# Kernel tuning notes

Measured on AMD Instinct MI355X. Metric: run time of the kernel, lower is better.

Reference implementation:

```python
import jax, jax.numpy as jnp
import numpy as np

D = 16      # input_dim (state dimension)
H = 64      # hidden width
B = 32768   # batch size


def setup_inputs() -> dict:
    key = jax.random.key(0)
    ks = jax.random.split(key, 16)
    inp = {
        "ts": jnp.arange(3, dtype=jnp.float32),          # output times [0, 1, 2]
        "x0": jax.random.normal(ks[0], (B, D), jnp.float32),
    }
    dims = [(D, H), (H, H), (H, H), (H, D)]
    i = 1
    for l, (din, dout) in enumerate(dims):
        inp[f"W{l}"] = jax.random.normal(ks[i], (din, dout), jnp.float32) / np.sqrt(din).astype(np.float32)
        inp[f"b{l}"] = jnp.zeros((dout,), jnp.float32)
        inp[f"g{l}"] = jax.random.normal(ks[i + 1], (dout,), jnp.float32) * 0.1   # hyper_gate weight (Linear(1,dout))
        inp[f"gb{l}"] = jnp.zeros((dout,), jnp.float32)                            # hyper_gate bias
        inp[f"hb{l}"] = jax.random.normal(ks[i + 2], (dout,), jnp.float32) * 0.1   # hyper_bias weight (no bias)
        i += 3
    return inp


def reference(ts, x0,
              W0, b0, g0, gb0, hb0,
              W1, b1, g1, gb1, hb1,
              W2, b2, g2, gb2, hb2,
              W3, b3, g3, gb3, hb3):
    layers = [(W0, b0, g0, gb0, hb0), (W1, b1, g1, gb1, hb1),
              (W2, b2, g2, gb2, hb2), (W3, b3, g3, gb3, hb3)]
    n_layers = len(layers)

    def odenet(t, x):
        # ConcatSquashLinear: (x@W + b) * sigmoid(t*g + gb) + t*hb, tanh between layers
        h = x
        for l, (W, b, g, gb, hb) in enumerate(layers):
            h = (h @ W + b) * jax.nn.sigmoid(t * g + gb) + t * hb
            if l < n_layers - 1:
                h = jnp.tanh(h)
        return h

    def odefunc(t, z):
        # z: [B, D+2]; last two channels accumulate log-det and kinetic energy
        x = z[:, :D]
        f = lambda xx: odenet(t, xx)
        dx = f(x)
        # exact divergence = trace of Jacobian, via D forward-mode JVPs
        eye = jnp.eye(D, dtype=x.dtype)
        Jv = jax.vmap(lambda e: jax.jvp(f, (x,), (jnp.broadcast_to(e, x.shape),))[1])(eye)  # [D, B, D]
        dl = jnp.einsum('ibi->b', Jv)                  # trace per sample
        dv = 0.5 * jnp.sum(dx * dx, axis=1)            # kinetic energy density
        return jnp.concatenate([dx, dl[:, None], dv[:, None]], axis=1)

    z0 = jnp.pad(x0, ((0, 0), (0, 2)))  # F.pad(x0, (0,2)) with zeros

    def rk4_step(z, t_pair):
        t0, t1 = t_pair
        h = t1 - t0
        k1 = odefunc(t0, z)
        k2 = odefunc(t0 + 0.5 * h, z + 0.5 * h * k1)
        k3 = odefunc(t0 + 0.5 * h, z + 0.5 * h * k2)
        k4 = odefunc(t1, z + h * k3)
        zn = z + (h / 6.0) * (k1 + 2.0 * k2 + 2.0 * k3 + k4)
        return zn, zn

    _, zs_tail = jax.lax.scan(rk4_step, z0, (ts[:-1], ts[1:]))
    zs = jnp.concatenate([z0[None], zs_tail], axis=0)   # [T, B, D+2]

    xs = zs[:, :, :-2]
    log_det = zs[-1, :, -2]
    loss_L = jnp.abs(zs[-1, :, -1])
    return xs, log_det, loss_L, jnp.zeros_like(loss_L)
```

## Files before the change

kernel.cpp:

```cpp
#include <hip/hip_runtime.h>

#define NB 32768
#define DD 16
#define HH 64
#define EPB 16

typedef __attribute__((ext_vector_type(8))) short short8;
typedef __attribute__((ext_vector_type(2))) float f32x2;
typedef __attribute__((ext_vector_type(4))) float f32x4;
typedef __attribute__((ext_vector_type(4))) unsigned uint4v;

union Frag { short8 s; uint4v u; unsigned d[4]; };

struct Params {
  const float *ts, *x0;
  const float *W0,*b0,*g0,*gb0,*hb0;
  const float *W1,*b1,*g1,*gb1,*hb1;
  const float *W2,*b2,*g2,*gb2,*hb2;
  const float *W3,*b3,*g3,*gb3,*hb3;
  float *out;
};

__device__ __forceinline__ unsigned short f2bf(float f){
  unsigned u=__float_as_uint(f);
  return (unsigned short)((u + 0x7FFFu + ((u>>16)&1u))>>16);
}
__device__ __forceinline__ unsigned pk2bf(float lo, float hi){
  unsigned a=__float_as_uint(lo)+0x8000u;
  unsigned b=__float_as_uint(hi)+0x8000u;
  return __builtin_amdgcn_perm(b, a, 0x07060302u);
}
__device__ __forceinline__ unsigned pk2bf2(f32x2 v){
  unsigned a=__float_as_uint(v[0])+0x8000u;
  unsigned b=__float_as_uint(v[1])+0x8000u;
  return __builtin_amdgcn_perm(b, a, 0x07060302u);
}
__device__ __forceinline__ unsigned short f2bf1(float f){
  return (unsigned short)((__float_as_uint(f)+0x8000u)>>16);
}
__device__ __forceinline__ float sigm(float u){
  return __builtin_amdgcn_rcpf(1.0f+__builtin_amdgcn_exp2f(-1.44269504f*u));
}
#define WV() __builtin_amdgcn_wave_barrier()
#define MFMA(A,B,C) __builtin_amdgcn_mfma_f32_16x16x32_bf16((A),(B),(C),0,0,0)

__device__ __forceinline__ void fwd_epi(const f32x4& c, float tcur,
    float gc, float gbc, float hbc,
    unsigned short* __restrict__ hdst, float* __restrict__ sdst,
    int jw, int q)
{
  const float gate = sigm(tcur*gc+gbc);
  const float gk   = gate*2.88539008f;
  const float tbk  = (tcur*hbc)*2.88539008f;
  const float g4   = 4.0f*gate;
  const f32x2 c01={c[0],c[1]}, c23={c[2],c[3]};
  const f32x2 pre01 = c01*gk + tbk;
  const f32x2 pre23 = c23*gk + tbk;
  const f32x2 e01={__builtin_amdgcn_exp2f(pre01[0]),__builtin_amdgcn_exp2f(pre01[1])};
  const f32x2 e23={__builtin_amdgcn_exp2f(pre23[0]),__builtin_amdgcn_exp2f(pre23[1])};
  const f32x2 d01=e01+1.0f, d23=e23+1.0f;
  const f32x2 rc01={__builtin_amdgcn_rcpf(d01[0]),__builtin_amdgcn_rcpf(d01[1])};
  const f32x2 rc23={__builtin_amdgcn_rcpf(d23[0]),__builtin_amdgcn_rcpf(d23[1])};
  const f32x2 th01 = rc01*-2.0f + 1.0f;
  const f32x2 th23 = rc23*-2.0f + 1.0f;
  const f32x2 om01 = 1.0f - rc01, om23 = 1.0f - rc23;
  const f32x2 sv01 = (rc01*g4)*om01, sv23 = (rc23*g4)*om23;
  const int el0=q*4;
  hdst[(el0+0)*72+jw]=f2bf1(th01[0]);
  hdst[(el0+1)*72+jw]=f2bf1(th01[1]);
  hdst[(el0+2)*72+jw]=f2bf1(th23[0]);
  hdst[(el0+3)*72+jw]=f2bf1(th23[1]);
  sdst[(el0+0)*68+jw]=sv01[0];
  sdst[(el0+1)*68+jw]=sv01[1];
  sdst[(el0+2)*68+jw]=sv23[0];
  sdst[(el0+3)*68+jw]=sv23[1];
}

__global__ __launch_bounds__(256,2) void traj_kernel(Params p){
  __shared__ __align__(16) unsigned short w0b[DD][72];
  __shared__ __align__(16) float w3tt[HH][20];
  __shared__ __align__(16) unsigned short xh[DD][40];
  __shared__ __align__(16) unsigned short xl[DD][40];
  __shared__ __align__(16) unsigned short hbh[2][EPB][72];
  __shared__ __align__(16) float sbf[3][EPB][68];
  __shared__ __align__(16) float sig3w[4][DD];
  __shared__ __align__(16) float dxs[4][4][17];
  __shared__ __align__(16) unsigned short vt[4][DD][72];

  const int tid = threadIdx.x;
  const int e   = tid>>4;
  const int a   = tid&15;
  const int wv  = tid>>6;
  const int lane= tid&63;
  const int m   = lane&15;
  const int q   = lane>>4;
  const int b   = blockIdx.x*EPB + e;
  const int jw  = wv*16 + m;

  short8 f0fr, f1fr[2], f2fr[2], b3fr[2];
  short8 b1fr[2][4], b2fr[2][4];
  {
    #pragma unroll
    for(int j=0;j<8;++j){
      const int k=q*8+j;
      f0fr[j]=(k<DD)?(short)f2bf(p.W0[k*HH+jw]):(short)0;
    }
    #pragma unroll
    for(int kk=0;kk<2;++kk){
      #pragma unroll
      for(int j=0;j<8;++j){
        const int k=kk*32+q*8+j;
        f1fr[kk][j]=(short)f2bf(p.W1[k*HH+jw]);
        f2fr[kk][j]=(short)f2bf(p.W2[k*HH+jw]);
        b3fr[kk][j]=(short)f2bf(p.W3[k*DD+m]);
      }
      #pragma unroll
      for(int nt=0;nt<4;++nt){
        #pragma unroll
        for(int j=0;j<8;++j){
          const int k=kk*32+q*8+j;
          b1fr[kk][nt][j]=(short)f2bf(p.W1[k*HH+4*m+nt]);
          b2fr[kk][nt][j]=(short)f2bf(p.W2[k*HH+4*m+nt]);
        }
      }
    }
  }
  const float bc0=p.b0[jw], gc0=p.g0[jw], gbc0=p.gb0[jw], hbc0=p.hb0[jw];
  const float bc1=p.b1[jw], gc1=p.g1[jw], gbc1=p.gb1[jw], hbc1=p.hb1[jw];
  const float bc2=p.b2[jw], gc2=p.g2[jw], gbc2=p.gb2[jw], hbc2=p.hb2[jw];
  const float bc3=p.b3[m],  gc3=p.g3[m],  gbc3=p.gb3[m],  hbc3=p.hb3[m];

  for(int idx=tid; idx<DD*HH; idx+=256) w0b[idx>>6][idx&63]=f2bf(p.W0[idx]);
  for(int idx=tid; idx<HH*DD; idx+=256) w3tt[idx>>4][idx&15]=p.W3[idx];
  if(tid<128){
    const int mm=tid>>3, dd=8+(tid&7);
    reinterpret_cast<unsigned*>(xh)[mm*20+dd]=0;
    reinterpret_cast<unsigned*>(xl)[mm*20+dd]=0;
  }
  __syncthreads();

  float zbx = p.x0[b*DD+a];
  p.out[b*DD+a]=zbx;
  float trp[4]={0.f,0.f,0.f,0.f};
  float dvp=0.f;

  #pragma unroll 1
  for(int step=0; step<2; ++step){
    const float t0=p.ts[step], t1=p.ts[step+1];
    const float hs=t1-t0;
    float dzx=0.f;
    float zwx=zbx;
    #pragma unroll 1
    for(int stage=0; stage<4; ++stage){
      const float cin=(stage==0)?0.f:((stage==3)?1.f:0.5f);
      const float tcur=t0+cin*hs;
      const float wg=(stage==0||stage==3)?1.f:2.f;
      const float fs=hs*(1.f/6.f)*wg;
      const float fs5=0.5f*fs;

      {
        const unsigned ux=__float_as_uint(zwx);
        xh[e][a]=(unsigned short)(ux>>16);
        xl[e][a]=f2bf1(zwx-__uint_as_float(ux&0xFFFF0000u));
      }
      __syncthreads();

      f32x4 c={bc0,bc0,bc0,bc0};
      {
        const short8 ah=*reinterpret_cast<const short8*>(&xh[m][q*8]);
        const short8 al=*reinterpret_cast<const short8*>(&xl[m][q*8]);
        c=MFMA(ah,f0fr,c); c=MFMA(al,f0fr,c);
      }
      fwd_epi(c,tcur,gc0,gbc0,hbc0,&hbh[0][0][0],&sbf[0][0][0],jw,q);
      __syncthreads();

      c=f32x4{bc1,bc1,bc1,bc1};
      #pragma unroll
      for(int kk=0;kk<2;++kk){
        const short8 ah=*reinterpret_cast<const short8*>(&hbh[0][m][kk*32+q*8]);
        c=MFMA(ah,f1fr[kk],c);
      }
      fwd_epi(c,tcur,gc1,gbc1,hbc1,&hbh[1][0][0],&sbf[1][0][0],jw,q);
      __syncthreads();

      c=f32x4{bc2,bc2,bc2,bc2};
      #pragma unroll
      for(int kk=0;kk<2;++kk){
        const short8 ah=*reinterpret_cast<const short8*>(&hbh[1][m][kk*32+q*8]);
        c=MFMA(ah,f2fr[kk],c);
      }
      fwd_epi(c,tcur,gc2,gbc2,hbc2,&hbh[0][0][0],&sbf[2][0][0],jw,q);
      __syncthreads();

      c=f32x4{bc3,bc3,bc3,bc3};
      #pragma unroll
      for(int kk=0;kk<2;++kk){
        const short8 ah=*reinterpret_cast<const short8*>(&hbh[0][m][kk*32+q*8]);
        c=MFMA(ah,b3fr[kk],c);
      }
      const float gate3=sigm(tcur*gc3+gbc3);
      const float tb3=tcur*hbc3;
      if(q==wv){
        #pragma unroll
        for(int r=0;r<4;++r)
          dxs[wv][r][m]=c[r]*gate3+tb3;
      }
      if(q==0) sig3w[wv][m]=gate3;
      WV();
      const float dxk=dxs[wv][q][m];
      dvp += fs5*dxk*dxk;

      f32x2 tf2[4][2];
      {
        const f32x4 sg4=*reinterpret_cast<const f32x4*>(&sig3w[wv][q*4]);
        const f32x2 sgA={sg4[0],sg4[1]}, sgB={sg4[2],sg4[3]};
        #pragma unroll
        for(int nt=0;nt<4;++nt){
          const f32x4 w4=*reinterpret_cast<const f32x4*>(&w3tt[4*m+nt][q*4]);
          tf2[nt][0]=sgA*f32x2{w4[0],w4[1]};
          tf2[nt][1]=sgB*f32x2{w4[2],w4[3]};
        }
      }

      #pragma unroll
      for(int el=0; el<4; ++el){
        const int ee=wv*4+el;
        Frag a0[2];
        #pragma unroll
        for(int kk=0;kk<2;++kk){
          const uint4v wd=*reinterpret_cast<const uint4v*>(&w0b[m][kk*32+q*8]);
          const f32x4 sA=*reinterpret_cast<const f32x4*>(&sbf[0][ee][kk*32+q*8]);
          const f32x4 sB=*reinterpret_cast<const f32x4*>(&sbf[0][ee][kk*32+q*8+4]);
          #pragma unroll
          for(int d=0;d<4;++d){
            const unsigned w2d=wd[d];
            const f32x2 w2={__uint_as_float(w2d<<16),__uint_as_float(w2d&0xFFFF0000u)};
            const f32x2 s2=(d<2)? f32x2{sA[2*d],sA[2*d+1]} : f32x2{sB[2*d-4],sB[2*d-3]};
            a0[kk].d[d]=pk2bf2(w2*s2);
          }
        }
        f32x4 c1[4]={{0,0,0,0},{0,0,0,0},{0,0,0,0},{0,0,0,0}};
        #pragma unroll
        for(int kk=0;kk<2;++kk){
          #pragma unroll
          for(int nt=0;nt<4;++nt)
            c1[nt]=MFMA(a0[kk].s,b1fr[kk][nt],c1[nt]);
        }
        {
          const f32x4 s1v=*reinterpret_cast<const f32x4*>(&sbf[1][ee][4*m]);
          const f32x4 pr0=c1[0]*s1v[0], pr1=c1[1]*s1v[1];
          const f32x4 pr2=c1[2]*s1v[2], pr3=c1[3]*s1v[3];
          #pragma unroll
          for(int r=0;r<4;++r){
            uint2 dw;
            dw.x=pk2bf(pr0[r],pr1[r]);
            dw.y=pk2bf(pr2[r],pr3[r]);
            *reinterpret_cast<uint2*>(&vt[wv][q*4+r][4*m])=dw;
          }
        }
        WV();
        short8 a2[2];
        #pragma unroll
        for(int kk=0;kk<2;++kk)
          a2[kk]=*reinterpret_cast<const short8*>(&vt[wv][m][kk*32+q*8]);
        f32x4 c2[4]={{0,0,0,0},{0,0,0,0},{0,0,0,0},{0,0,0,0}};
        #pragma unroll
        for(int kk=0;kk<2;++kk){
          #pragma unroll
          for(int nt=0;nt<4;++nt)
            c2[nt]=MFMA(a2[kk],b2fr[kk][nt],c2[nt]);
        }
        {
          const f32x4 s2v=*reinterpret_cast<const f32x4*>(&sbf[2][ee][4*m]);
          float tr=0.f;
          #pragma unroll
          for(int nt=0;nt<4;++nt){
            const f32x2 t = f32x2{c2[nt][0],c2[nt][1]}*tf2[nt][0]
                          + f32x2{c2[nt][2],c2[nt][3]}*tf2[nt][1];
            tr += (t[0]+t[1])*s2v[nt];
          }
          trp[el] += fs*tr;
        }
        WV();
      }

      dzx += fs*dxk;
      const float cn=(stage==2)?1.f:0.5f;
      if(stage<3) zwx=zbx+cn*hs*dxk;
    }
    zbx += dzx;
    p.out[(step+1)*(NB*DD)+b*DD+a]=zbx;
  }

  #pragma unroll
  for(int el=0; el<4; ++el){
    float v=trp[el];
    #pragma unroll
    for(int mk=32;mk>=1;mk>>=1) v+=__shfl_xor(v,mk,64);
    if(lane==el) p.out[3*NB*DD + blockIdx.x*EPB + wv*4 + el]=v;
  }
  {
    float v=dvp;
    #pragma unroll
    for(int mk=8;mk>=1;mk>>=1) v+=__shfl_xor(v,mk,16);
    if(a==0){
      p.out[3*NB*DD+NB+b]=fabsf(v);
      p.out[3*NB*DD+2*NB+b]=0.f;
    }
  }
}

extern "C" void kernel_launch(void* const* d_in, const int* in_sizes, int n_in,
                              void* d_out, int out_size, void* d_ws, size_t ws_size,
                              hipStream_t stream){
  Params p;
  p.ts  = (const float*)d_in[0];
  p.x0  = (const float*)d_in[1];
  p.W0  = (const float*)d_in[2];  p.b0 =(const float*)d_in[3];
  p.g0  = (const float*)d_in[4];  p.gb0=(const float*)d_in[5];  p.hb0=(const float*)d_in[6];
  p.W1  = (const float*)d_in[7];  p.b1 =(const float*)d_in[8];
  p.g1  = (const float*)d_in[9];  p.gb1=(const float*)d_in[10]; p.hb1=(const float*)d_in[11];
  p.W2  = (const float*)d_in[12]; p.b2 =(const float*)d_in[13];
  p.g2  = (const float*)d_in[14]; p.gb2=(const float*)d_in[15]; p.hb2=(const float*)d_in[16];
  p.W3  = (const float*)d_in[17]; p.b3 =(const float*)d_in[18];
  p.g3  = (const float*)d_in[19]; p.gb3=(const float*)d_in[20]; p.hb3=(const float*)d_in[21];
  p.out = (float*)d_out;
  hipLaunchKernelGGL(traj_kernel, dim3(NB/EPB), dim3(256), 0, stream, p);
}
```

Baseline: 246.8 us.

## Move layer-0/3 weight fragments and per-layer scalars to LDS; raise occupancy to 3

The W0 and W3 MFMA B-fragments and the per-layer gate/bias scalars now live in shared memory and are reloaded each stage, instead of being held in registers for the whole kernel. The Jacobian MFMA chains are split into two pairs of accumulators so fewer accumulator registers are live at once. Launch bounds go from 2 to 3 blocks per CU. The aim is to cut VGPR pressure enough to fit more waves per CU, at the cost of extra LDS reads and more LDS use per block.

```diff
diff --git a/kernel.cpp b/kernel.cpp
--- a/kernel.cpp
+++ b/kernel.cpp
@@ -45,13 +45,13 @@
 #define MFMA(A,B,C) __builtin_amdgcn_mfma_f32_16x16x32_bf16((A),(B),(C),0,0,0)
 
 __device__ __forceinline__ void fwd_epi(const f32x4& c, float tcur,
-    float gc, float gbc, float hbc,
+    const float4 sc,
     unsigned short* __restrict__ hdst, float* __restrict__ sdst,
     int jw, int q)
 {
-  const float gate = sigm(tcur*gc+gbc);
+  const float gate = sigm(tcur*sc.x+sc.y);
   const float gk   = gate*2.88539008f;
-  const float tbk  = (tcur*hbc)*2.88539008f;
+  const float tbk  = (tcur*sc.z)*2.88539008f;
   const float g4   = 4.0f*gate;
   const f32x2 c01={c[0],c[1]}, c23={c[2],c[3]};
   const f32x2 pre01 = c01*gk + tbk;
@@ -76,9 +76,13 @@
   sdst[(el0+3)*68+jw]=sv23[1];
 }
 
-__global__ __launch_bounds__(256,2) void traj_kernel(Params p){
+__global__ __launch_bounds__(256,3) void traj_kernel(Params p){
   __shared__ __align__(16) unsigned short w0b[DD][72];
   __shared__ __align__(16) float w3tt[HH][20];
+  __shared__ __align__(16) unsigned short w0t[HH][32];
+  __shared__ __align__(16) unsigned short b3f[2][64][8];
+  __shared__ __align__(16) float4 lscA[3][64];
+  __shared__ __align__(16) float4 lsc3[16];
   __shared__ __align__(16) unsigned short xh[DD][40];
   __shared__ __align__(16) unsigned short xl[DD][40];
   __shared__ __align__(16) unsigned short hbh[2][EPB][72];
@@ -97,14 +101,9 @@
   const int b   = blockIdx.x*EPB + e;
   const int jw  = wv*16 + m;
 
-  short8 f0fr, f1fr[2], f2fr[2], b3fr[2];
+  short8 f1fr[2], f2fr[2];
   short8 b1fr[2][4], b2fr[2][4];
   {
-    #pragma unroll
-    for(int j=0;j<8;++j){
-      const int k=q*8+j;
-      f0fr[j]=(k<DD)?(short)f2bf(p.W0[k*HH+jw]):(short)0;
-    }
     #pragma unroll
     for(int kk=0;kk<2;++kk){
       #pragma unroll
@@ -112,7 +111,6 @@
         const int k=kk*32+q*8+j;
         f1fr[kk][j]=(short)f2bf(p.W1[k*HH+jw]);
         f2fr[kk][j]=(short)f2bf(p.W2[k*HH+jw]);
-        b3fr[kk][j]=(short)f2bf(p.W3[k*DD+m]);
       }
       #pragma unroll
       for(int nt=0;nt<4;++nt){
@@ -125,13 +123,22 @@
       }
     }
   }
-  const float bc0=p.b0[jw], gc0=p.g0[jw], gbc0=p.gb0[jw], hbc0=p.hb0[jw];
-  const float bc1=p.b1[jw], gc1=p.g1[jw], gbc1=p.gb1[jw], hbc1=p.hb1[jw];
-  const float bc2=p.b2[jw], gc2=p.g2[jw], gbc2=p.gb2[jw], hbc2=p.hb2[jw];
-  const float bc3=p.b3[m],  gc3=p.g3[m],  gbc3=p.gb3[m],  hbc3=p.hb3[m];
 
   for(int idx=tid; idx<DD*HH; idx+=256) w0b[idx>>6][idx&63]=f2bf(p.W0[idx]);
   for(int idx=tid; idx<HH*DD; idx+=256) w3tt[idx>>4][idx&15]=p.W3[idx];
+  for(int idx=tid; idx<HH*32; idx+=256){
+    const int c_=idx>>5, k=idx&31;
+    w0t[c_][k] = (k<DD) ? f2bf(p.W0[k*HH+c_]) : (unsigned short)0;
+  }
+  for(int idx=tid; idx<1024; idx+=256){
+    const int kk=idx>>9, ln=(idx>>3)&63, j=idx&7;
+    const int k=kk*32+(ln>>4)*8+j;
+    b3f[kk][ln][j]=f2bf(p.W3[k*DD+(ln&15)]);
+  }
+  if(tid<64)            lscA[0][tid]    =make_float4(p.g0[tid],p.gb0[tid],p.hb0[tid],p.b0[tid]);
+  else if(tid<128)      lscA[1][tid-64] =make_float4(p.g1[tid-64],p.gb1[tid-64],p.hb1[tid-64],p.b1[tid-64]);
+  else if(tid<192)      lscA[2][tid-128]=make_float4(p.g2[tid-128],p.gb2[tid-128],p.hb2[tid-128],p.b2[tid-128]);
+  else if(tid<208)      lsc3[tid-192]   =make_float4(p.g3[tid-192],p.gb3[tid-192],p.hb3[tid-192],p.b3[tid-192]);
   if(tid<128){
     const int mm=tid>>3, dd=8+(tid&7);
     reinterpret_cast<unsigned*>(xh)[mm*20+dd]=0;
@@ -165,41 +172,47 @@
       }
       __syncthreads();
 
-      f32x4 c={bc0,bc0,bc0,bc0};
+      float4 sc0=lscA[0][jw];
+      f32x4 c={sc0.w,sc0.w,sc0.w,sc0.w};
       {
+        const short8 f0fr=*reinterpret_cast<const short8*>(&w0t[jw][q*8]);
         const short8 ah=*reinterpret_cast<const short8*>(&xh[m][q*8]);
         const short8 al=*reinterpret_cast<const short8*>(&xl[m][q*8]);
         c=MFMA(ah,f0fr,c); c=MFMA(al,f0fr,c);
       }
-      fwd_epi(c,tcur,gc0,gbc0,hbc0,&hbh[0][0][0],&sbf[0][0][0],jw,q);
+      fwd_epi(c,tcur,sc0,&hbh[0][0][0],&sbf[0][0][0],jw,q);
       __syncthreads();
 
-      c=f32x4{bc1,bc1,bc1,bc1};
+      float4 sc1=lscA[1][jw];
+      c=f32x4{sc1.w,sc1.w,sc1.w,sc1.w};
       #pragma unroll
       for(int kk=0;kk<2;++kk){
         const short8 ah=*reinterpret_cast<const short8*>(&hbh[0][m][kk*32+q*8]);
         c=MFMA(ah,f1fr[kk],c);
       }
-      fwd_epi(c,tcur,gc1,gbc1,hbc1,&hbh[1][0][0],&sbf[1][0][0],jw,q);
+      fwd_epi(c,tcur,sc1,&hbh[1][0][0],&sbf[1][0][0],jw,q);
       __syncthreads();
 
-      c=f32x4{bc2,bc2,bc2,bc2};
+      float4 sc2=lscA[2][jw];
+      c=f32x4{sc2.w,sc2.w,sc2.w,sc2.w};
       #pragma unroll
       for(int kk=0;kk<2;++kk){
         const short8 ah=*reinterpret_cast<const short8*>(&hbh[1][m][kk*32+q*8]);
         c=MFMA(ah,f2fr[kk],c);
       }
-      fwd_epi(c,tcur,gc2,gbc2,hbc2,&hbh[0][0][0],&sbf[2][0][0],jw,q);
+      fwd_epi(c,tcur,sc2,&hbh[0][0][0],&sbf[2][0][0],jw,q);
       __syncthreads();
 
-      c=f32x4{bc3,bc3,bc3,bc3};
+      float4 sc3=lsc3[m];
+      c=f32x4{sc3.w,sc3.w,sc3.w,sc3.w};
       #pragma unroll
       for(int kk=0;kk<2;++kk){
+        const short8 bf3=*reinterpret_cast<const short8*>(&b3f[kk][lane][0]);
         const short8 ah=*reinterpret_cast<const short8*>(&hbh[0][m][kk*32+q*8]);
-        c=MFMA(ah,b3fr[kk],c);
-      }
-      const float gate3=sigm(tcur*gc3+gbc3);
-      const float tb3=tcur*hbc3;
+        c=MFMA(ah,bf3,c);
+      }
+      const float gate3=sigm(tcur*sc3.x+sc3.y);
+      const float tb3=tcur*sc3.z;
       if(q==wv){
         #pragma unroll
         for(int r=0;r<4;++r)
@@ -239,48 +252,40 @@
             a0[kk].d[d]=pk2bf2(w2*s2);
           }
         }
-        f32x4 c1[4]={{0,0,0,0},{0,0,0,0},{0,0,0,0},{0,0,0,0}};
-        #pragma unroll
-        for(int kk=0;kk<2;++kk){
+        #pragma unroll
+        for(int np=0; np<2; ++np){
+          f32x4 cA={0,0,0,0}, cB={0,0,0,0};
           #pragma unroll
-          for(int nt=0;nt<4;++nt)
-            c1[nt]=MFMA(a0[kk].s,b1fr[kk][nt],c1[nt]);
-        }
-        {
-          const f32x4 s1v=*reinterpret_cast<const f32x4*>(&sbf[1][ee][4*m]);
-          const f32x4 pr0=c1[0]*s1v[0], pr1=c1[1]*s1v[1];
-          const f32x4 pr2=c1[2]*s1v[2], pr3=c1[3]*s1v[3];
+          for(int kk=0;kk<2;++kk){
+            cA=MFMA(a0[kk].s,b1fr[kk][2*np  ],cA);
+            cB=MFMA(a0[kk].s,b1fr[kk][2*np+1],cB);
+          }
+          const f32x2 s1v=*reinterpret_cast<const f32x2*>(&sbf[1][ee][4*m+2*np]);
+          const f32x4 prA=cA*s1v[0], prB=cB*s1v[1];
           #pragma unroll
-          for(int r=0;r<4;++r){
-            uint2 dw;
-            dw.x=pk2bf(pr0[r],pr1[r]);
-            dw.y=pk2bf(pr2[r],pr3[r]);
-            *reinterpret_cast<uint2*>(&vt[wv][q*4+r][4*m])=dw;
-          }
+          for(int r=0;r<4;++r)
+            *reinterpret_cast<unsigned*>(&vt[wv][q*4+r][4*m+2*np])=pk2bf(prA[r],prB[r]);
         }
         WV();
         short8 a2[2];
         #pragma unroll
         for(int kk=0;kk<2;++kk)
           a2[kk]=*reinterpret_cast<const short8*>(&vt[wv][m][kk*32+q*8]);
-        f32x4 c2[4]={{0,0,0,0},{0,0,0,0},{0,0,0,0},{0,0,0,0}};
-        #pragma unroll
-        for(int kk=0;kk<2;++kk){
+        float tr=0.f;
+        #pragma unroll
+        for(int np=0; np<2; ++np){
+          f32x4 cA={0,0,0,0}, cB={0,0,0,0};
           #pragma unroll
-          for(int nt=0;nt<4;++nt)
-            c2[nt]=MFMA(a2[kk],b2fr[kk][nt],c2[nt]);
-        }
-        {
-          const f32x4 s2v=*reinterpret_cast<const f32x4*>(&sbf[2][ee][4*m]);
-          float tr=0.f;
-          #pragma unroll
-          for(int nt=0;nt<4;++nt){
-            const f32x2 t = f32x2{c2[nt][0],c2[nt][1]}*tf2[nt][0]
-                          + f32x2{c2[nt][2],c2[nt][3]}*tf2[nt][1];
-            tr += (t[0]+t[1])*s2v[nt];
+          for(int kk=0;kk<2;++kk){
+            cA=MFMA(a2[kk],b2fr[kk][2*np  ],cA);
+            cB=MFMA(a2[kk],b2fr[kk][2*np+1],cB);
           }
-          trp[el] += fs*tr;
-        }
+          const f32x2 s2v=*reinterpret_cast<const f32x2*>(&sbf[2][ee][4*m+2*np]);
+          const f32x2 tA = f32x2{cA[0],cA[1]}*tf2[2*np  ][0] + f32x2{cA[2],cA[3]}*tf2[2*np  ][1];
+          const f32x2 tB = f32x2{cB[0],cB[1]}*tf2[2*np+1][0] + f32x2{cB[2],cB[3]}*tf2[2*np+1][1];
+          tr += (tA[0]+tA[1])*s2v[0] + (tB[0]+tB[1])*s2v[1];
+        }
+        trp[el] += fs*tr;
         WV();
       }
 
```

New measurement: 259.0 us. 4.9% more time.
